# Kernel optimization log

Hardware: AMD Instinct MI355X
Metric: run time of the kernel (lower is better)

## Reference

```python
import jax, jax.numpy as jnp
import numpy as np


def setup_inputs() -> dict:
    key = jax.random.key(0)
    k1, k2 = jax.random.split(key)
    B, T, D = 32, 512, 512
    encoder_output = jax.random.normal(k1, (B, T, D), dtype=jnp.float32)
    durations = jax.random.randint(k2, (B, T), 0, 8, dtype=jnp.int32)
    return {"encoder_output": encoder_output, "durations": durations, "t_out": 4096}


def reference(encoder_output, durations, t_out):
    # Faithful to the TF loop: duration = max(dur, 1); repeat each phoneme
    # vector `duration` times along time; pad to fixed length t_out with zeros.
    B, T, D = encoder_output.shape
    dur = jnp.maximum(durations.astype(jnp.int32), 1)        # [B, T]
    ends = jnp.cumsum(dur, axis=1)                            # [B, T] cumulative end frame per phoneme
    pos = jnp.arange(t_out, dtype=jnp.int32)                  # [t_out] output frame indices
    # For frame j, source phoneme = first t with ends[t] > j  (searchsorted right)
    idx = jax.vmap(lambda e: jnp.searchsorted(e, pos, side='right'))(ends)  # [B, t_out]
    valid = pos[None, :] < ends[:, -1:]                       # frames past total length -> zero pad
    idx = jnp.minimum(idx, T - 1)
    out = jnp.take_along_axis(encoder_output, idx[:, :, None], axis=1)      # [B, t_out, D]
    return out * valid[:, :, None].astype(encoder_output.dtype)
```

## Files before the change

kernel.cpp:

```cpp
#include <hip/hip_runtime.h>


#define T_PH 512
#define FPB  16

typedef float f32x4 __attribute__((ext_vector_type(4)));

__global__ __launch_bounds__(256) void lr_fused_kernel(
    const f32x4* __restrict__ enc,
    const int*   __restrict__ dur,
    f32x4*       __restrict__ out,
    int t_out) {

    __shared__ int e[T_PH];
    __shared__ int wtot[4];
    __shared__ int idxs[FPB];

    const int tid  = threadIdx.x;
    const int wav  = tid >> 6;
    const int lane = tid & 63;
    const int b    = blockIdx.y;
    const int j0   = blockIdx.x * FPB;

    int2 d2 = ((const int2*)(dur + b * T_PH))[tid];
    int v0 = (d2.x < 1) ? 1 : d2.x;
    int v1 = (d2.y < 1) ? 1 : d2.y;
    int p  = v0 + v1;

    #pragma unroll
    for (int off = 1; off < 64; off <<= 1) {
        int t = __shfl_up(p, off);
        if (lane >= off) p += t;
    }
    if (lane == 63) wtot[wav] = p;
    __syncthreads();

    int wbase = 0;
    #pragma unroll
    for (int w = 0; w < 3; ++w)
        wbase += (wav > w) ? wtot[w] : 0;
    int S = wbase + p;
    e[2 * tid]     = S - v1;
    e[2 * tid + 1] = S;
    __syncthreads();

    const int total = e[T_PH - 1];

    if (tid < FPB) {
        int j = j0 + tid;
        int r;
        if (j >= total) {
            r = -1;
        } else {
            int lo = 0, hi = T_PH - 1;
            while (lo < hi) {
                int mid = (lo + hi) >> 1;
                if (e[mid] <= j) lo = mid + 1; else hi = mid;
            }
            r = lo;
        }
        idxs[tid] = r;
    }
    __syncthreads();

    const int lane128 = tid & 127;
    const int fh      = tid >> 7;

    const f32x4* __restrict__ encb = enc + (size_t)b * T_PH * 128;
    f32x4* __restrict__ outb = out + ((size_t)b * t_out + j0) * 128 + lane128;

    const f32x4 zero = {0.f, 0.f, 0.f, 0.f};

    int pi[8];
    #pragma unroll
    for (int k = 0; k < 8; ++k) pi[k] = idxs[fh + 2 * k];

    f32x4 w[8];
    #pragma unroll
    for (int k = 0; k < 8; ++k)
        w[k] = (pi[k] >= 0) ? encb[(size_t)pi[k] * 128 + lane128] : zero;

    #pragma unroll
    for (int k = 0; k < 8; ++k)
        __builtin_nontemporal_store(w[k], &outb[(size_t)(fh + 2 * k) * 128]);
}

extern "C" void kernel_launch(void* const* d_in, const int* in_sizes, int n_in,
                              void* d_out, int out_size, void* d_ws, size_t ws_size,
                              hipStream_t stream) {
    const float* enc = (const float*)d_in[0];
    const int* dur   = (const int*)d_in[1];
    float* out       = (float*)d_out;

    const int BT = in_sizes[1];
    const int T  = T_PH;
    const int B  = BT / T;
    const int D  = in_sizes[0] / BT;
    const int t_out = out_size / (B * D);

    dim3 grid(t_out / FPB, B);
    lr_fused_kernel<<<grid, 256, 0, stream>>>(
        (const f32x4*)enc, dur, (f32x4*)out, t_out);
}
```

Before: 54.10 us.

## Replace binary search with scatter of phoneme indices and halve frames per block

Each thread now scatters its two phonemes' indices directly into the per-block frame index table, using its prefix-sum intervals. This replaces the shared cumsum array and the per-frame binary search, and drops one barrier. Frames per block go from 16 to 8, which doubles the grid and repeats the duration scan across twice as many blocks. Frames past the total length stay at -1 from initialisation and are zero-filled.

```diff
diff --git a/kernel.cpp b/kernel.cpp
--- a/kernel.cpp
+++ b/kernel.cpp
@@ -2,7 +2,7 @@
 
 
 #define T_PH 512
-#define FPB  16
+#define FPB  8
 
 typedef float f32x4 __attribute__((ext_vector_type(4)));
 
@@ -12,7 +12,6 @@
     f32x4*       __restrict__ out,
     int t_out) {
 
-    __shared__ int e[T_PH];
     __shared__ int wtot[4];
     __shared__ int idxs[FPB];
 
@@ -33,6 +32,7 @@
         if (lane >= off) p += t;
     }
     if (lane == 63) wtot[wav] = p;
+    if (tid < FPB) idxs[tid] = -1;
     __syncthreads();
 
     int wbase = 0;
@@ -40,26 +40,16 @@
     for (int w = 0; w < 3; ++w)
         wbase += (wav > w) ? wtot[w] : 0;
     int S = wbase + p;
-    e[2 * tid]     = S - v1;
-    e[2 * tid + 1] = S;
-    __syncthreads();
 
-    const int total = e[T_PH - 1];
-
-    if (tid < FPB) {
-        int j = j0 + tid;
-        int r;
-        if (j >= total) {
-            r = -1;
-        } else {
-            int lo = 0, hi = T_PH - 1;
-            while (lo < hi) {
-                int mid = (lo + hi) >> 1;
-                if (e[mid] <= j) lo = mid + 1; else hi = mid;
-            }
-            r = lo;
-        }
-        idxs[tid] = r;
+    {
+        int s0 = S - v1 - v0, e0 = S - v1;
+        int lo = (s0 > j0) ? s0 : j0;
+        int hi = (e0 < j0 + FPB) ? e0 : (j0 + FPB);
+        for (int j = lo; j < hi; ++j) idxs[j - j0] = 2 * tid;
+        int s1 = e0, e1 = S;
+        lo = (s1 > j0) ? s1 : j0;
+        hi = (e1 < j0 + FPB) ? e1 : (j0 + FPB);
+        for (int j = lo; j < hi; ++j) idxs[j - j0] = 2 * tid + 1;
     }
     __syncthreads();
 
@@ -71,18 +61,20 @@
 
     const f32x4 zero = {0.f, 0.f, 0.f, 0.f};
 
-    int pi[8];
-    #pragma unroll
-    for (int k = 0; k < 8; ++k) pi[k] = idxs[fh + 2 * k];
+    int p0 = idxs[fh + 0];
+    int p1 = idxs[fh + 2];
+    int p2 = idxs[fh + 4];
+    int p3 = idxs[fh + 6];
 
-    f32x4 w[8];
-    #pragma unroll
-    for (int k = 0; k < 8; ++k)
-        w[k] = (pi[k] >= 0) ? encb[(size_t)pi[k] * 128 + lane128] : zero;
+    f32x4 w0 = (p0 >= 0) ? encb[(size_t)p0 * 128 + lane128] : zero;
+    f32x4 w1 = (p1 >= 0) ? encb[(size_t)p1 * 128 + lane128] : zero;
+    f32x4 w2 = (p2 >= 0) ? encb[(size_t)p2 * 128 + lane128] : zero;
+    f32x4 w3 = (p3 >= 0) ? encb[(size_t)p3 * 128 + lane128] : zero;
 
-    #pragma unroll
-    for (int k = 0; k < 8; ++k)
-        __builtin_nontemporal_store(w[k], &outb[(size_t)(fh + 2 * k) * 128]);
+    __builtin_nontemporal_store(w0, &outb[(size_t)(fh + 0) * 128]);
+    __builtin_nontemporal_store(w1, &outb[(size_t)(fh + 2) * 128]);
+    __builtin_nontemporal_store(w2, &outb[(size_t)(fh + 4) * 128]);
+    __builtin_nontemporal_store(w3, &outb[(size_t)(fh + 6) * 128]);
 }
 
 extern "C" void kernel_launch(void* const* d_in, const int* in_sizes, int n_in,
```

After: 51.47 us. -4.8%, faster.
